# Optimization experiments

Hardware: AMD Instinct MI355X
Metric: run time of the kernel (lower is better)

The kernel has to match this reference:

```python
import jax, jax.numpy as jnp
import numpy as np

D_MODEL = 1024
NUM_HEADS = 16
D_K = D_MODEL // NUM_HEADS
B, S = 2, 2048
LN_EPS = 1e-5


def setup_inputs() -> dict:
    key = jax.random.key(0)
    ks = jax.random.split(key, 11)
    sc = 1.0 / np.sqrt(D_MODEL)
    return {
        "x": jax.random.normal(ks[0], (B, S, D_MODEL), dtype=jnp.float32),
        "Wq": jax.random.normal(ks[1], (D_MODEL, D_MODEL), dtype=jnp.float32) * sc,
        "bq": jnp.zeros((D_MODEL,), dtype=jnp.float32),
        "Wk": jax.random.normal(ks[2], (D_MODEL, D_MODEL), dtype=jnp.float32) * sc,
        "bk": jnp.zeros((D_MODEL,), dtype=jnp.float32),
        "Wv": jax.random.normal(ks[3], (D_MODEL, D_MODEL), dtype=jnp.float32) * sc,
        "bv": jnp.zeros((D_MODEL,), dtype=jnp.float32),
        "Wo": jax.random.normal(ks[4], (D_MODEL, D_MODEL), dtype=jnp.float32) * sc,
        "bo": jnp.zeros((D_MODEL,), dtype=jnp.float32),
        "ln_gamma": jnp.ones((D_MODEL,), dtype=jnp.float32),
        "ln_beta": jnp.zeros((D_MODEL,), dtype=jnp.float32),
    }


def reference(x, Wq, bq, Wk, bk, Wv, bv, Wo, bo, ln_gamma, ln_beta):
    b, s, d = x.shape
    # QKV projections -> [B, H, S, D_K]
    def split_heads(y):
        return y.reshape(b, s, NUM_HEADS, D_K).transpose(0, 2, 1, 3)
    q = split_heads(x @ Wq + bq)
    k = split_heads(x @ Wk + bk)
    v = split_heads(x @ Wv + bv)
    # scores [B, H, S, S]; dropout is identity in eval mode
    scores = jnp.einsum("bhqd,bhkd->bhqk", q, k) / jnp.sqrt(jnp.float32(D_K))
    attn = jax.nn.softmax(scores, axis=-1)
    context = jnp.einsum("bhqk,bhkd->bhqd", attn, v)
    context = context.transpose(0, 2, 1, 3).reshape(b, s, d)
    out = context @ Wo + bo
    # residual + LayerNorm (eps=1e-5, torch default)
    h = x + out
    mu = jnp.mean(h, axis=-1, keepdims=True)
    var = jnp.var(h, axis=-1, keepdims=True)
    return (h - mu) / jnp.sqrt(var + LN_EPS) * ln_gamma + ln_beta
```

## Files before the change

### kernel.cpp

```cpp
#include <hip/hip_runtime.h>
#include <math.h>

#define D_MODEL 1024
#define NHEAD   16
#define DKK     64
#define BATCH   2
#define SEQ     2048
#define MROWS   (BATCH*SEQ)

typedef __attribute__((ext_vector_type(8)))  short bf16x8;
typedef __attribute__((ext_vector_type(4)))  short bf16x4;
typedef __attribute__((ext_vector_type(4)))  float f32x4;
typedef __attribute__((ext_vector_type(16))) float f32x16;

#define MFMA(a,b,c)   __builtin_amdgcn_mfma_f32_16x16x32_bf16((a),(b),(c),0,0,0)
#define MFMA32(a,b,c) __builtin_amdgcn_mfma_f32_32x32x16_bf16((a),(b),(c),0,0,0)

#define QSCALE 0.18033688f

#define SBAR() { __builtin_amdgcn_sched_barrier(0); \
                 __builtin_amdgcn_s_barrier();      \
                 __builtin_amdgcn_sched_barrier(0); }

#define CH  520
#define TIL (8*CH)

__device__ __forceinline__ short f2b(float f) {
    unsigned u = __float_as_uint(f);
    unsigned r = (u + 0x7FFFu + ((u >> 16) & 1u)) >> 16;
    return (short)r;
}

__device__ __forceinline__ float fexp2(float x) {
    float r; asm("v_exp_f32 %0, %1" : "=v"(r) : "v"(x)); return r;
}

__device__ __forceinline__ void gld_lds16(const void* g, void* l) {
    __builtin_amdgcn_global_load_lds(
        (const __attribute__((address_space(1))) void*)g,
        (__attribute__((address_space(3))) void*)l, 16, 0, 0);
}

__global__ __launch_bounds__(256)
void prep_weights(const float* __restrict__ Wq, const float* __restrict__ Wk,
                  const float* __restrict__ Wv, const float* __restrict__ Wo,
                  short* __restrict__ wt3, short* __restrict__ wot)
{
    const int z = blockIdx.z;
    const float* W = z==0 ? Wq : z==1 ? Wk : z==2 ? Wv : Wo;
    short* dst = (z < 3) ? (wt3 + (size_t)z*1024*1024) : wot;
    __shared__ float tile[32][33];
    const int tx = threadIdx.x & 31, ty = threadIdx.x >> 5;
    const int c0 = blockIdx.x*32, r0 = blockIdx.y*32;
    #pragma unroll
    for (int i = 0; i < 4; i++)
        tile[ty + i*8][tx] = W[(size_t)(r0 + ty + i*8)*1024 + c0 + tx];
    __syncthreads();
    #pragma unroll
    for (int i = 0; i < 4; i++)
        dst[(size_t)(c0 + ty + i*8)*1024 + r0 + tx] = f2b(tile[tx][ty + i*8]);
}

__global__ __launch_bounds__(256)
void convert_x(const float* __restrict__ x, short* __restrict__ xb)
{
    const int i = (blockIdx.x*256 + threadIdx.x) * 8;
    float4 a = *(const float4*)(x + i);
    float4 c = *(const float4*)(x + i + 4);
    bf16x8 v;
    v[0]=f2b(a.x); v[1]=f2b(a.y); v[2]=f2b(a.z); v[3]=f2b(a.w);
    v[4]=f2b(c.x); v[5]=f2b(c.y); v[6]=f2b(c.z); v[7]=f2b(c.w);
    *(bf16x8*)(xb + i) = v;
}

__global__ __launch_bounds__(512, 2)
void gemm_qkv(const short* __restrict__ A, const short* __restrict__ Bt,
              const float* __restrict__ bq, const float* __restrict__ bk,
              const float* __restrict__ bv,
              short* __restrict__ qb, short* __restrict__ kb, short* __restrict__ vtb)
{
    __shared__ short Ab[2*16384];
    __shared__ short Bb[2*12288];

    const int t = threadIdx.x;
    const int w = t >> 6, lane = t & 63;
    const int r = lane & 15, g4 = lane >> 4;
    const int wm = w >> 2, wn = w & 3;

    const int bid = blockIdx.x;
    const int xcd = bid & 7, idx = bid >> 3;
    const int mi  = (xcd >> 1) * 4 + (idx & 3);
    const int ni  = (xcd & 1) * 8 + (idx >> 2);
    const int m0 = mi * 256, n0 = ni * 192;

    const int srow = t >> 3;
    const int scol = ((t & 7) ^ (srow & 7)) * 8;

    f32x4 acc[8][3] = {};
    bf16x8 bfr[2][3];

#define QKV_STAGE(P, KT)                                                      \
    { const int kk = (KT) * 64 + scol;                                        \
      _Pragma("unroll")                                                       \
      for (int a = 0; a < 4; a++)                                             \
          gld_lds16(A + (size_t)(m0 + a*64 + srow)*1024 + kk,                 \
                    Ab + (P)*16384 + a*4096 + t*8);                           \
      _Pragma("unroll")                                                       \
      for (int p2 = 0; p2 < 3; p2++)                                          \
          gld_lds16(Bt + (size_t)(n0 + p2*64 + srow)*1024 + kk,               \
                    Bb + (P)*12288 + p2*4096 + t*8); }

#define QKV_PHASE(P, MH, KS, LOADB)                                           \
    { const short* Abase = Ab + (P)*16384 + wm*8192;                          \
      bf16x8 af[4];                                                           \
      _Pragma("unroll")                                                       \
      for (int i = 0; i < 4; i++)                                             \
          af[i] = *(const bf16x8*)&Abase[((MH)*64 + i*16 + r)*64 +            \
                                         (((KS)*4 + g4) ^ (r&7))*8];          \
      if (LOADB) {                                                            \
          const short* Bbase = Bb + (P)*12288;                                \
          _Pragma("unroll")                                                   \
          for (int j = 0; j < 3; j++)                                         \
              bfr[KS][j] = *(const bf16x8*)&Bbase[(wn*48 + j*16 + r)*64 +     \
                                                  (((KS)*4 + g4) ^ (r&7))*8]; \
      }                                                                       \
      SBAR();                                                                 \
      __builtin_amdgcn_s_setprio(1);                                          \
      _Pragma("unroll")                                                       \
      for (int i = 0; i < 4; i++)                                             \
          _Pragma("unroll")                                                   \
          for (int j = 0; j < 3; j++)                                         \
              acc[(MH)*4+i][j] = MFMA(af[i], bfr[KS][j], acc[(MH)*4+i][j]);   \
      __builtin_amdgcn_s_setprio(0);                                          \
      SBAR(); }

    QKV_STAGE(0, 0)
    QKV_STAGE(1, 1)
    asm volatile("s_waitcnt vmcnt(7)" ::: "memory");
    __builtin_amdgcn_s_barrier();
    __builtin_amdgcn_sched_barrier(0);

    int p = 0;
    #pragma unroll 1
    for (int kt = 0; kt < 16; kt++) {
        QKV_PHASE(p, 0, 0, 1)
        QKV_PHASE(p, 1, 0, 0)
        QKV_PHASE(p, 0, 1, 1)
        QKV_PHASE(p, 1, 1, 0)
        if (kt < 14) {
            QKV_STAGE(p, kt + 2)
            asm volatile("s_waitcnt vmcnt(7)" ::: "memory");
        } else {
            asm volatile("s_waitcnt vmcnt(0)" ::: "memory");
        }
        __builtin_amdgcn_s_barrier();
        __builtin_amdgcn_sched_barrier(0);
        p ^= 1;
    }
#undef QKV_STAGE
#undef QKV_PHASE

    #pragma unroll
    for (int n = 0; n < 3; n++) {
        const int colbase = n0 + wn*48 + n*16;
        const int proj    = colbase >> 10;
        const int within  = colbase & 1023;
        const int h       = within >> 6;
        const int d       = (within & 63) + r;
        const float* bias = (proj == 0) ? bq : (proj == 1) ? bk : bv;
        const float bval  = bias[within + r];
        #pragma unroll
        for (int m = 0; m < 8; m++) {
            const int growb = m0 + wm*128 + m*16 + g4*4;
            const int bidx  = growb >> 11;
            const int s     = growb & 2047;
            if (proj == 0) {
                #pragma unroll
                for (int i = 0; i < 4; i++)
                    qb[((size_t)(bidx*NHEAD + h)*SEQ + s + i)*DKK + d] =
                        f2b((acc[m][n][i] + bval) * QSCALE);
            } else if (proj == 1) {
                #pragma unroll
                for (int i = 0; i < 4; i++)
                    kb[((size_t)(bidx*NHEAD + h)*SEQ + s + i)*DKK + d] =
                        f2b(acc[m][n][i] + bval);
            } else {
                bf16x4 pk;
                #pragma unroll
                for (int i = 0; i < 4; i++) pk[i] = f2b(acc[m][n][i] + bval);
                *(bf16x4*)(vtb + ((size_t)(bidx*NHEAD + h)*DKK + d)*SEQ + s) = pk;
            }
        }
    }
}

__global__ __launch_bounds__(256)
void gemm_out(const short* __restrict__ A, const short* __restrict__ Bt,
              const float* __restrict__ bo, const float* __restrict__ resid,
              float* __restrict__ hb)
{
    __shared__ short As[2*128*32];
    __shared__ short Bs[2*64*32];
    const int t = threadIdx.x;
    const int w = t >> 6, lane = t & 63;
    const int r = lane & 15, g4 = lane >> 4;
    const int wr = w >> 1, wc = w & 1;

    const int bid = blockIdx.x;
    const int xcd = bid & 7, idx = bid >> 3;
    const int mi  = (xcd >> 1) * 8 + (idx & 7);
    const int ni  = (xcd & 1) * 8 + (idx >> 3);
    const int m0 = mi * 128, n0 = ni * 64;

    const int srow = lane >> 2, su = lane & 3;

    f32x4 acc[4][2] = {};

#define OUT_STAGE(BUF, K0)                                                     \
    { const int kk = (K0) & 1023;                                              \
      _Pragma("unroll")                                                        \
      for (int c = 0; c < 2; c++) {                                            \
          const int row = w*32 + c*16 + srow;                                  \
          gld_lds16(A + (size_t)(m0+row)*1024 + kk + 8*(su ^ ((row>>1)&3)),    \
                    As + (BUF)*4096 + w*1024 + c*512);                         \
      }                                                                        \
      { const int row = w*16 + srow;                                           \
        gld_lds16(Bt + (size_t)(n0+row)*1024 + kk + 8*(su ^ ((row>>1)&3)),     \
                  Bs + (BUF)*2048 + w*512); } }

    OUT_STAGE(0, 0)
    __syncthreads();

    int cur = 0;
    #pragma unroll 1
    for (int k0 = 0; k0 < 1024; k0 += 32) {
        OUT_STAGE(cur^1, k0 + 32)
        const short* Abase = As + cur*4096;
        const short* Bbase = Bs + cur*2048;
        bf16x8 af[4], bfr[2];
        #pragma unroll
        for (int m = 0; m < 4; m++) {
            const int row = wr*64 + m*16 + r;
            af[m] = *(const bf16x8*)&Abase[row*32 + (g4 ^ ((row>>1)&3))*8];
        }
        #pragma unroll
        for (int n = 0; n < 2; n++) {
            const int row = wc*32 + n*16 + r;
            bfr[n] = *(const bf16x8*)&Bbase[row*32 + (g4 ^ ((row>>1)&3))*8];
        }
        __builtin_amdgcn_s_setprio(1);
        #pragma unroll
        for (int m = 0; m < 4; m++)
            #pragma unroll
            for (int n = 0; n < 2; n++)
                acc[m][n] = MFMA(af[m], bfr[n], acc[m][n]);
        __builtin_amdgcn_s_setprio(0);
        __syncthreads();
        cur ^= 1;
    }
#undef OUT_STAGE

    #pragma unroll
    for (int n = 0; n < 2; n++) {
        const int col = n0 + wc*32 + n*16 + r;
        const float bval = bo[col];
        #pragma unroll
        for (int m = 0; m < 4; m++) {
            #pragma unroll
            for (int i = 0; i < 4; i++) {
                const int grow = m0 + wr*64 + m*16 + g4*4 + i;
                const size_t ofs = (size_t)grow*1024 + col;
                hb[ofs] = acc[m][n][i] + bval + resid[ofs];
            }
        }
    }
}

__global__ __launch_bounds__(256, 2)
void attn_mfma(const short* __restrict__ Q, const short* __restrict__ K,
               const short* __restrict__ VT, short* __restrict__ ctx)
{
    __shared__ short Ks[4*TIL];
    __shared__ short Vs[4*TIL];

    const int t = threadIdx.x;
    const int w = t >> 6, lane = t & 63;
    const int l31 = lane & 31, hi = lane >> 5;
    const int srow8 = lane >> 3, su = lane & 7;
    const int lane8 = lane * 8;
    const int swz8  = (su ^ srow8) * 8;

    const int bid     = blockIdx.x;
    const int logical = (bid & 7) * 64 + (bid >> 3);
    const int bh_lin  = logical >> 4;
    const int qt      = logical & 15;
    const int b = bh_lin >> 4, h = bh_lin & 15;
    const int q0 = qt * 128 + w * 32;

    const size_t bh = (size_t)b * NHEAD + h;
    const short* Qp = Q  + bh * SEQ * DKK;
    const short* Kp = K  + bh * SEQ * DKK;
    const short* Vp = VT + bh * DKK * SEQ;

    const short* kstage = Kp + (size_t)(w*8 + srow8) * DKK + swz8;
    const short* vstage = Vp + (size_t)(w*8 + srow8) * SEQ + swz8;

    bf16x8 qf[4];
    #pragma unroll
    for (int d0 = 0; d0 < 4; d0++)
        qf[d0] = *(const bf16x8*)(Qp + (size_t)(q0 + l31)*DKK + d0*16 + hi*8);

    int koff[8], voff[8];
    #pragma unroll
    for (int i = 0; i < 8; i++) {
        const int kchunk = (i>>2)*4 + (l31>>3);
        koff[i] = kchunk*CH + (l31&7)*64 + ((((i&3)*2 + hi) ^ (l31&7)) * 8);
        const int vchunk = (i&1)*4 + (l31>>3);
        voff[i] = vchunk*CH + (l31&7)*64 + ((((i>>1)*2 + hi) ^ (l31&7)) * 8);
    }

    f32x16 o0A = {}, o1A = {}, o0B = {}, o1B = {};
    float lrow = 0.f;

#define ATT_STAGE(KDST, VDST, J)                                               \
    { const size_t jj = (size_t)((J) & (SEQ-1));                               \
      const short* ksrc = kstage + jj*DKK;                                     \
      gld_lds16(ksrc,           (KDST) + w*CH + lane8);                        \
      gld_lds16(ksrc + 32*DKK,  (KDST) + (4+w)*CH + lane8);                    \
      const short* vsrc = vstage + jj;                                         \
      gld_lds16(vsrc,           (VDST) + w*CH + lane8);                        \
      gld_lds16(vsrc + 32*SEQ,  (VDST) + (4+w)*CH + lane8); }

#define QK_SUB(KB, S0, S1)                                                     \
    { bf16x8 kf[8];                                                            \
      _Pragma("unroll")                                                        \
      for (int i = 0; i < 8; i++) kf[i] = *(const bf16x8*)&(KB)[koff[i]];      \
      _Pragma("unroll")                                                        \
      for (int d0 = 0; d0 < 4; d0++) S0 = MFMA32(kf[d0],   qf[d0], S0);        \
      _Pragma("unroll")                                                        \
      for (int d0 = 0; d0 < 4; d0++) S1 = MFMA32(kf[4+d0], qf[d0], S1); }

#define PV_SUB(S0, S1, VB, O0, O1)                                             \
    { bf16x8 vf[8];                                                            \
      _Pragma("unroll")                                                        \
      for (int i = 0; i < 8; i++) vf[i] = *(const bf16x8*)&(VB)[voff[i]];      \
      _Pragma("unroll")                                                        \
      for (int ks = 0; ks < 4; ks++) {                                         \
        const int g = (ks & 1) * 8;                                            \
        float e0,e1,e2,e3,e4,e5,e6,e7;                                         \
        if (ks < 2) { e0=S0[g+0];e1=S0[g+1];e2=S0[g+2];e3=S0[g+3];             \
                      e4=S0[g+4];e5=S0[g+5];e6=S0[g+6];e7=S0[g+7]; }           \
        else        { e0=S1[g+0];e1=S1[g+1];e2=S1[g+2];e3=S1[g+3];             \
                      e4=S1[g+4];e5=S1[g+5];e6=S1[g+6];e7=S1[g+7]; }           \
        unsigned u0,u1,u2,u3;                                                  \
        asm("v_cvt_pk_bf16_f32 %0, %1, %2" : "=v"(u0) : "v"(e0), "v"(e1));     \
        asm("v_cvt_pk_bf16_f32 %0, %1, %2" : "=v"(u1) : "v"(e2), "v"(e3));     \
        asm("v_cvt_pk_bf16_f32 %0, %1, %2" : "=v"(u2) : "v"(e4), "v"(e5));     \
        asm("v_cvt_pk_bf16_f32 %0, %1, %2" : "=v"(u3) : "v"(e6), "v"(e7));     \
        auto rA = __builtin_amdgcn_permlane32_swap(u0, u2, false, false);      \
        auto rB = __builtin_amdgcn_permlane32_swap(u1, u3, false, false);      \
        union { unsigned u[4]; bf16x8 v; } pa;                                 \
        pa.u[0] = rA[0]; pa.u[1] = rB[0]; pa.u[2] = rA[1]; pa.u[3] = rB[1];    \
        O0 = MFMA32(pa.v, vf[ks*2+0], O0);                                     \
        O1 = MFMA32(pa.v, vf[ks*2+1], O1);                                     \
      } }

    ATT_STAGE(Ks,       Vs,       0)
    ATT_STAGE(Ks + TIL, Vs + TIL, 64)
    __syncthreads();

    int cur = 0;
    #pragma unroll 1
    for (int j0 = 0; j0 < SEQ; j0 += 128) {
        {
            const int nb = (cur^1)*2*TIL;
            ATT_STAGE(Ks + nb,       Vs + nb,       j0 + 128)
            ATT_STAGE(Ks + nb + TIL, Vs + nb + TIL, j0 + 192)
        }

        const short* KbA = Ks + cur*2*TIL;
        const short* VbA = Vs + cur*2*TIL;
        const short* KbB = KbA + TIL;
        const short* VbB = VbA + TIL;

        f32x16 s0A = {}, s1A = {}, s0B = {}, s1B = {};
        QK_SUB(KbA, s0A, s1A)
        QK_SUB(KbB, s0B, s1B)

        #pragma unroll
        for (int r = 0; r < 16; r++) s0A[r] = fexp2(s0A[r]);
        #pragma unroll
        for (int r = 0; r < 16; r++) s1A[r] = fexp2(s1A[r]);
        #pragma unroll
        for (int r = 0; r < 16; r++) s0B[r] = fexp2(s0B[r]);
        #pragma unroll
        for (int r = 0; r < 16; r++) s1B[r] = fexp2(s1B[r]);

        float ts[16];
        #pragma unroll
        for (int r = 0; r < 16; r++) ts[r] = (s0A[r] + s1A[r]) + (s0B[r] + s1B[r]);
        #pragma unroll
        for (int dd = 8; dd >= 1; dd >>= 1)
            #pragma unroll
            for (int r = 0; r < dd; r++) ts[r] += ts[r + dd];
        lrow += ts[0] + __shfl_xor(ts[0], 32);

        PV_SUB(s0A, s1A, VbA, o0A, o1A)
        PV_SUB(s0B, s1B, VbB, o0B, o1B)

        __syncthreads();
        cur ^= 1;
    }

    const float li = 1.f / lrow;
    const int lb = __float_as_int(li);
    #pragma unroll
    for (int r = 0; r < 16; r++) {
        const int crow = (r&3) + 8*(r>>2) + 4*hi;
        const float lv = __int_as_float(__builtin_amdgcn_ds_bpermute(crow*4, lb));
        const size_t base = ((size_t)b*SEQ + q0 + crow)*D_MODEL + h*DKK + l31;
        ctx[base]      = f2b((o0A[r] + o0B[r]) * lv);
        ctx[base + 32] = f2b((o1A[r] + o1B[r]) * lv);
    }
#undef ATT_STAGE
#undef QK_SUB
#undef PV_SUB
}

__global__ __launch_bounds__(256)
void ln_kernel(const float* __restrict__ hbuf, const float* __restrict__ gamma,
               const float* __restrict__ beta, float* __restrict__ out)
{
    const int row = blockIdx.x;
    const int t = threadIdx.x;
    const float* hp = hbuf + (size_t)row * D_MODEL;
    float4 v = ((const float4*)hp)[t];
    float sum = v.x + v.y + v.z + v.w;
    float sq  = v.x*v.x + v.y*v.y + v.z*v.z + v.w*v.w;
    #pragma unroll
    for (int o = 1; o <= 32; o <<= 1) {
        sum += __shfl_xor(sum, o);
        sq  += __shfl_xor(sq, o);
    }
    __shared__ float s1[4], s2[4];
    if ((t & 63) == 0) { s1[t >> 6] = sum; s2[t >> 6] = sq; }
    __syncthreads();
    sum = s1[0] + s1[1] + s1[2] + s1[3];
    sq  = s2[0] + s2[1] + s2[2] + s2[3];
    const float mean = sum * (1.0f / D_MODEL);
    const float var  = sq * (1.0f / D_MODEL) - mean * mean;
    const float inv  = rsqrtf(var + 1e-5f);
    float4 g  = ((const float4*)gamma)[t];
    float4 be = ((const float4*)beta)[t];
    float4 rr;
    rr.x = (v.x - mean) * inv * g.x + be.x;
    rr.y = (v.y - mean) * inv * g.y + be.y;
    rr.z = (v.z - mean) * inv * g.z + be.z;
    rr.w = (v.w - mean) * inv * g.w + be.w;
    ((float4*)(out + (size_t)row * D_MODEL))[t] = rr;
}

extern "C" void kernel_launch(void* const* d_in, const int* in_sizes, int n_in,
                              void* d_out, int out_size, void* d_ws, size_t ws_size,
                              hipStream_t stream)
{
    const float* x  = (const float*)d_in[0];
    const float* Wq = (const float*)d_in[1];
    const float* bq = (const float*)d_in[2];
    const float* Wk = (const float*)d_in[3];
    const float* bk = (const float*)d_in[4];
    const float* Wv = (const float*)d_in[5];
    const float* bv = (const float*)d_in[6];
    const float* Wo = (const float*)d_in[7];
    const float* bo = (const float*)d_in[8];
    const float* g  = (const float*)d_in[9];
    const float* be = (const float*)d_in[10];

    short* xb  = (short*)d_ws;
    short* wt3 = xb  + (size_t)4096*1024;
    short* wot = wt3 + (size_t)3072*1024;
    short* qb  = wot + (size_t)1024*1024;
    short* kb  = qb  + (size_t)4096*1024;
    short* vtb = kb  + (size_t)4096*1024;
    short* cxb = vtb + (size_t)4096*1024;
    float* hb  = (float*)(cxb + (size_t)4096*1024);

    prep_weights<<<dim3(32,32,4), 256, 0, stream>>>(Wq, Wk, Wv, Wo, wt3, wot);
    convert_x  <<<2048, 256, 0, stream>>>(x, xb);
    gemm_qkv   <<<256, 512, 0, stream>>>(xb, wt3, bq, bk, bv, qb, kb, vtb);
    attn_mfma  <<<512, 256, 0, stream>>>(qb, kb, vtb, cxb);
    gemm_out   <<<512, 256, 0, stream>>>(cxb, wot, bo, x, hb);
    ln_kernel  <<<MROWS, 256, 0, stream>>>(hb, g, be, (float*)d_out);
}
```

Before: 122.6 us.

## Double query rows per attention wave to reuse K/V fragments

Each wave now processes 64 query rows, as two 32-row groups, instead of 32. The K and V fragments read from LDS are shared across both groups, and the grid shrinks to 256 blocks of 256 queries each. This halves LDS reads and global K/V staging per query, but it raises register pressure, so launch bounds drop to one block per SIMD slot and occupancy falls. MFMA sections are wrapped in s_setprio raises to favour matrix issue.

```diff
diff --git a/kernel.cpp b/kernel.cpp
--- a/kernel.cpp
+++ b/kernel.cpp
@@ -276,7 +276,7 @@
     }
 }
 
-__global__ __launch_bounds__(256, 2)
+__global__ __launch_bounds__(256, 1)
 void attn_mfma(const short* __restrict__ Q, const short* __restrict__ K,
                const short* __restrict__ VT, short* __restrict__ ctx)
 {
@@ -291,11 +291,11 @@
     const int swz8  = (su ^ srow8) * 8;
 
     const int bid     = blockIdx.x;
-    const int logical = (bid & 7) * 64 + (bid >> 3);
-    const int bh_lin  = logical >> 4;
-    const int qt      = logical & 15;
+    const int logical = (bid & 7) * 32 + (bid >> 3);
+    const int bh_lin  = logical >> 3;
+    const int qt      = logical & 7;
     const int b = bh_lin >> 4, h = bh_lin & 15;
-    const int q0 = qt * 128 + w * 32;
+    const int q0 = qt * 256 + w * 64;
 
     const size_t bh = (size_t)b * NHEAD + h;
     const short* Qp = Q  + bh * SEQ * DKK;
@@ -305,10 +305,12 @@
     const short* kstage = Kp + (size_t)(w*8 + srow8) * DKK + swz8;
     const short* vstage = Vp + (size_t)(w*8 + srow8) * SEQ + swz8;
 
-    bf16x8 qf[4];
-    #pragma unroll
-    for (int d0 = 0; d0 < 4; d0++)
-        qf[d0] = *(const bf16x8*)(Qp + (size_t)(q0 + l31)*DKK + d0*16 + hi*8);
+    bf16x8 qfA[4], qfB[4];
+    #pragma unroll
+    for (int d0 = 0; d0 < 4; d0++) {
+        qfA[d0] = *(const bf16x8*)(Qp + (size_t)(q0      + l31)*DKK + d0*16 + hi*8);
+        qfB[d0] = *(const bf16x8*)(Qp + (size_t)(q0 + 32 + l31)*DKK + d0*16 + hi*8);
+    }
 
     int koff[8], voff[8];
     #pragma unroll
@@ -319,8 +321,8 @@
         voff[i] = vchunk*CH + (l31&7)*64 + ((((i>>1)*2 + hi) ^ (l31&7)) * 8);
     }
 
-    f32x16 o0A = {}, o1A = {}, o0B = {}, o1B = {};
-    float lrow = 0.f;
+    f32x16 oA0 = {}, oA1 = {}, oB0 = {}, oB1 = {};
+    float lrowA = 0.f, lrowB = 0.f;
 
 #define ATT_STAGE(KDST, VDST, J)                                               \
     { const size_t jj = (size_t)((J) & (SEQ-1));                               \
@@ -331,19 +333,19 @@
       gld_lds16(vsrc,           (VDST) + w*CH + lane8);                        \
       gld_lds16(vsrc + 32*SEQ,  (VDST) + (4+w)*CH + lane8); }
 
-#define QK_SUB(KB, S0, S1)                                                     \
-    { bf16x8 kf[8];                                                            \
-      _Pragma("unroll")                                                        \
-      for (int i = 0; i < 8; i++) kf[i] = *(const bf16x8*)&(KB)[koff[i]];      \
-      _Pragma("unroll")                                                        \
-      for (int d0 = 0; d0 < 4; d0++) S0 = MFMA32(kf[d0],   qf[d0], S0);        \
-      _Pragma("unroll")                                                        \
-      for (int d0 = 0; d0 < 4; d0++) S1 = MFMA32(kf[4+d0], qf[d0], S1); }
-
-#define PV_SUB(S0, S1, VB, O0, O1)                                             \
-    { bf16x8 vf[8];                                                            \
-      _Pragma("unroll")                                                        \
-      for (int i = 0; i < 8; i++) vf[i] = *(const bf16x8*)&(VB)[voff[i]];      \
+#define SOFTMAX_PA(S0, S1, LROW, PA)                                           \
+    { _Pragma("unroll")                                                        \
+      for (int r = 0; r < 16; r++) S0[r] = fexp2(S0[r]);                       \
+      _Pragma("unroll")                                                        \
+      for (int r = 0; r < 16; r++) S1[r] = fexp2(S1[r]);                       \
+      float ts[16];                                                            \
+      _Pragma("unroll")                                                        \
+      for (int r = 0; r < 16; r++) ts[r] = S0[r] + S1[r];                      \
+      _Pragma("unroll")                                                        \
+      for (int dd = 8; dd >= 1; dd >>= 1)                                      \
+          _Pragma("unroll")                                                    \
+          for (int r = 0; r < dd; r++) ts[r] += ts[r + dd];                    \
+      LROW += ts[0];                                                           \
       _Pragma("unroll")                                                        \
       for (int ks = 0; ks < 4; ks++) {                                         \
         const int g = (ks & 1) * 8;                                            \
@@ -361,9 +363,46 @@
         auto rB = __builtin_amdgcn_permlane32_swap(u1, u3, false, false);      \
         union { unsigned u[4]; bf16x8 v; } pa;                                 \
         pa.u[0] = rA[0]; pa.u[1] = rB[0]; pa.u[2] = rA[1]; pa.u[3] = rB[1];    \
-        O0 = MFMA32(pa.v, vf[ks*2+0], O0);                                     \
-        O1 = MFMA32(pa.v, vf[ks*2+1], O1);                                     \
+        PA[ks] = pa.v;                                                         \
       } }
+
+#define SUBTILE(KB, VB)                                                        \
+    { bf16x8 kf[8];                                                            \
+      _Pragma("unroll")                                                        \
+      for (int i = 0; i < 8; i++) kf[i] = *(const bf16x8*)&(KB)[koff[i]];      \
+      bf16x8 paA[4], paB[4];                                                   \
+      {                                                                        \
+        f32x16 s0 = {}, s1 = {};                                               \
+        __builtin_amdgcn_s_setprio(1);                                         \
+        _Pragma("unroll")                                                      \
+        for (int d0 = 0; d0 < 4; d0++) s0 = MFMA32(kf[d0],   qfA[d0], s0);     \
+        _Pragma("unroll")                                                      \
+        for (int d0 = 0; d0 < 4; d0++) s1 = MFMA32(kf[4+d0], qfA[d0], s1);     \
+        __builtin_amdgcn_s_setprio(0);                                         \
+        SOFTMAX_PA(s0, s1, lrowA, paA)                                         \
+      }                                                                        \
+      {                                                                        \
+        f32x16 s0 = {}, s1 = {};                                               \
+        __builtin_amdgcn_s_setprio(1);                                         \
+        _Pragma("unroll")                                                      \
+        for (int d0 = 0; d0 < 4; d0++) s0 = MFMA32(kf[d0],   qfB[d0], s0);     \
+        _Pragma("unroll")                                                      \
+        for (int d0 = 0; d0 < 4; d0++) s1 = MFMA32(kf[4+d0], qfB[d0], s1);     \
+        __builtin_amdgcn_s_setprio(0);                                         \
+        SOFTMAX_PA(s0, s1, lrowB, paB)                                         \
+      }                                                                        \
+      bf16x8 vf[8];                                                            \
+      _Pragma("unroll")                                                        \
+      for (int i = 0; i < 8; i++) vf[i] = *(const bf16x8*)&(VB)[voff[i]];      \
+      __builtin_amdgcn_s_setprio(1);                                           \
+      _Pragma("unroll")                                                        \
+      for (int ks = 0; ks < 4; ks++) {                                         \
+          oA0 = MFMA32(paA[ks], vf[ks*2+0], oA0);                              \
+          oA1 = MFMA32(paA[ks], vf[ks*2+1], oA1);                              \
+          oB0 = MFMA32(paB[ks], vf[ks*2+0], oB0);                              \
+          oB1 = MFMA32(paB[ks], vf[ks*2+1], oB1);                              \
+      }                                                                        \
+      __builtin_amdgcn_s_setprio(0); }
 
     ATT_STAGE(Ks,       Vs,       0)
     ATT_STAGE(Ks + TIL, Vs + TIL, 64)
@@ -380,51 +419,35 @@
 
         const short* KbA = Ks + cur*2*TIL;
         const short* VbA = Vs + cur*2*TIL;
-        const short* KbB = KbA + TIL;
-        const short* VbB = VbA + TIL;
-
-        f32x16 s0A = {}, s1A = {}, s0B = {}, s1B = {};
-        QK_SUB(KbA, s0A, s1A)
-        QK_SUB(KbB, s0B, s1B)
-
-        #pragma unroll
-        for (int r = 0; r < 16; r++) s0A[r] = fexp2(s0A[r]);
-        #pragma unroll
-        for (int r = 0; r < 16; r++) s1A[r] = fexp2(s1A[r]);
-        #pragma unroll
-        for (int r = 0; r < 16; r++) s0B[r] = fexp2(s0B[r]);
-        #pragma unroll
-        for (int r = 0; r < 16; r++) s1B[r] = fexp2(s1B[r]);
-
-        float ts[16];
-        #pragma unroll
-        for (int r = 0; r < 16; r++) ts[r] = (s0A[r] + s1A[r]) + (s0B[r] + s1B[r]);
-        #pragma unroll
-        for (int dd = 8; dd >= 1; dd >>= 1)
-            #pragma unroll
-            for (int r = 0; r < dd; r++) ts[r] += ts[r + dd];
-        lrow += ts[0] + __shfl_xor(ts[0], 32);
-
-        PV_SUB(s0A, s1A, VbA, o0A, o1A)
-        PV_SUB(s0B, s1B, VbB, o0B, o1B)
+
+        SUBTILE(KbA,        VbA)
+        SUBTILE(KbA + TIL,  VbA + TIL)
 
         __syncthreads();
         cur ^= 1;
     }
 
-    const float li = 1.f / lrow;
-    const int lb = __float_as_int(li);
-    #pragma unroll
-    for (int r = 0; r < 16; r++) {
-        const int crow = (r&3) + 8*(r>>2) + 4*hi;
-        const float lv = __int_as_float(__builtin_amdgcn_ds_bpermute(crow*4, lb));
-        const size_t base = ((size_t)b*SEQ + q0 + crow)*D_MODEL + h*DKK + l31;
-        ctx[base]      = f2b((o0A[r] + o0B[r]) * lv);
-        ctx[base + 32] = f2b((o1A[r] + o1B[r]) * lv);
+    {
+        const float lA = lrowA + __shfl_xor(lrowA, 32);
+        const float lB = lrowB + __shfl_xor(lrowB, 32);
+        const int lbA = __float_as_int(1.f / lA);
+        const int lbB = __float_as_int(1.f / lB);
+        #pragma unroll
+        for (int r = 0; r < 16; r++) {
+            const int crow = (r&3) + 8*(r>>2) + 4*hi;
+            const float lvA = __int_as_float(__builtin_amdgcn_ds_bpermute(crow*4, lbA));
+            const float lvB = __int_as_float(__builtin_amdgcn_ds_bpermute(crow*4, lbB));
+            const size_t baseA = ((size_t)b*SEQ + q0 + crow)*D_MODEL + h*DKK + l31;
+            const size_t baseB = ((size_t)b*SEQ + q0 + 32 + crow)*D_MODEL + h*DKK + l31;
+            ctx[baseA]      = f2b(oA0[r] * lvA);
+            ctx[baseA + 32] = f2b(oA1[r] * lvA);
+            ctx[baseB]      = f2b(oB0[r] * lvB);
+            ctx[baseB + 32] = f2b(oB1[r] * lvB);
+        }
     }
 #undef ATT_STAGE
-#undef QK_SUB
-#undef PV_SUB
+#undef SOFTMAX_PA
+#undef SUBTILE
 }
 
 __global__ __launch_bounds__(256)
@@ -488,7 +511,7 @@
     prep_weights<<<dim3(32,32,4), 256, 0, stream>>>(Wq, Wk, Wv, Wo, wt3, wot);
     convert_x  <<<2048, 256, 0, stream>>>(x, xb);
     gemm_qkv   <<<256, 512, 0, stream>>>(xb, wt3, bq, bk, bv, qb, kb, vtb);
-    attn_mfma  <<<512, 256, 0, stream>>>(qb, kb, vtb, cxb);
+    attn_mfma  <<<256, 256, 0, stream>>>(qb, kb, vtb, cxb);
     gemm_out   <<<512, 256, 0, stream>>>(cxb, wot, bo, x, hb);
     ln_kernel  <<<MROWS, 256, 0, stream>>>(hb, g, be, (float*)d_out);
 }
```

Measured after the change: 130.4 us. +6.4%, slower.
